# Kernel tuning notes

Hardware: AMD Instinct MI355X
Metric: run time of the kernel (lower is better)

Reference implementation:

```python
import jax, jax.numpy as jnp
import numpy as np

B, T, D, L = 64, 512, 1024, 32


def setup_inputs() -> dict:
    key = jax.random.key(0)
    ks = jax.random.split(key, 6)
    x = jax.random.normal(ks[0], (B, T, D), jnp.float32)
    W = jax.random.normal(ks[1], (D, L), jnp.float32) * 0.02  # TruncatedNormal(stddev=0.02) analogue
    b = jnp.zeros((L,), jnp.float32)
    transitions = jax.random.normal(ks[2], (L, L), jnp.float32) * 0.1
    label = jax.random.randint(ks[3], (B, T), 0, L).astype(jnp.int32)
    seqlen = jax.random.randint(ks[4], (B,), 1, T + 1).astype(jnp.int32)
    mask = jnp.arange(T)[None, :] < seqlen[:, None]
    return {"x": x, "W": W, "b": b, "transitions": transitions,
            "label": label, "seqlen": seqlen, "mask": mask}


def crf_sequence_score(emissions, label, seqlen, transitions):
    # emissions: [B,T,L]
    Bc, Tc, Lc = emissions.shape
    m = (jnp.arange(Tc)[None, :] < seqlen[:, None]).astype(emissions.dtype)  # [B,T]
    unary = jnp.take_along_axis(emissions, label[..., None].astype(jnp.int32), axis=-1)[..., 0]
    unary = jnp.sum(unary * m, axis=1)
    trans = transitions[label[:, :-1], label[:, 1:]]  # [B,T-1]
    mt = (jnp.arange(1, Tc)[None, :] < seqlen[:, None]).astype(emissions.dtype)
    binary = jnp.sum(trans * mt, axis=1)
    return unary + binary


def crf_log_norm(emissions, seqlen, transitions):
    Bc, Tc, Lc = emissions.shape
    alpha0 = emissions[:, 0]  # [B,L]
    valid = (jnp.arange(1, Tc)[None, :] < seqlen[:, None]).T  # [T-1,B]
    emits = jnp.moveaxis(emissions[:, 1:], 1, 0)  # [T-1,B,L]

    def step(alpha, inp):
        emit_t, v = inp
        new = jax.nn.logsumexp(alpha[:, :, None] + transitions[None], axis=1) + emit_t
        return jnp.where(v[:, None], new, alpha), None

    alpha, _ = jax.lax.scan(step, alpha0, (emits, valid))
    return jax.nn.logsumexp(alpha, axis=-1)  # [B]


def crf_decode(emissions, transitions, seqlen):
    Bc, Tc, Lc = emissions.shape
    alpha0 = emissions[:, 0]
    idx = jnp.arange(Lc, dtype=jnp.int32)
    valid = (jnp.arange(1, Tc)[None, :] < seqlen[:, None]).T  # [T-1,B]
    emits = jnp.moveaxis(emissions[:, 1:], 1, 0)

    def fwd(alpha, inp):
        emit_t, v = inp
        scores = alpha[:, :, None] + transitions[None]  # [B,L,L]
        best = jnp.max(scores, axis=1) + emit_t
        bp = jnp.argmax(scores, axis=1).astype(jnp.int32)  # [B,L]
        alpha_new = jnp.where(v[:, None], best, alpha)
        bp = jnp.where(v[:, None], bp, idx[None, :])  # identity bp on padded steps
        return alpha_new, bp

    alpha, bps = jax.lax.scan(fwd, alpha0, (emits, valid))  # bps: [T-1,B,L]
    last = jnp.argmax(alpha, axis=-1).astype(jnp.int32)  # [B]

    def bwd(tag, bp):
        prev = jnp.take_along_axis(bp, tag[:, None], axis=1)[:, 0]
        return prev, tag

    first, tags = jax.lax.scan(bwd, last, bps, reverse=True)  # tags[i] = tag at t=i+1
    seq = jnp.concatenate([first[None], tags], axis=0)  # [T,B]
    return jnp.moveaxis(seq, 0, 1)  # [B,T]


def reference(x, W, b, transitions, label, seqlen, mask):
    emissions = jnp.einsum('btd,dl->btl', x, W) + b  # Dense projection
    ll = crf_sequence_score(emissions, label, seqlen, transitions) - crf_log_norm(emissions, seqlen, transitions)
    loss = jnp.mean(-ll)
    vit = crf_decode(emissions, transitions, seqlen)
    tp = jnp.sum(((label > 0) & (vit == label)).astype(jnp.float32))
    tn = jnp.sum(((label > 0) & (vit != label)).astype(jnp.float32))
    fp = jnp.sum((mask & (label == 0) & (vit > 0)).astype(jnp.float32))
    return loss, vit, tp, tn, fp
```

## Files before the change

### kernel.cpp

```cpp
#include <hip/hip_runtime.h>
#include <stdint.h>
#include <math.h>

#define Bn 64
#define Tn 512
#define Dn 1024
#define Ln 32
#define LOG2E 1.4426950408889634f
#define LN2f  0.6931471805599453f

#define EMIS_OFF 0
#define LOGNORM_OFF (Bn * Tn * Ln)
#define SCORE_OFF (LOGNORM_OFF + Bn)
#define CNT_OFF (SCORE_OFF + Bn)

#define MAX3(a,b,c) fmaxf(fmaxf((a),(b)),(c))

__device__ __forceinline__ void half_swap(float p, float& x, float& y) {
    x = p; y = p;
    asm volatile("v_permlane32_swap_b32 %0, %1" : "+v"(x), "+v"(y));
}

#define BM 128
#define KB 32
#define XSS 132

__global__ __launch_bounds__(256) void gemm_emis(
    const float* __restrict__ x, const float* __restrict__ Wm,
    const float* __restrict__ bias, const int* __restrict__ seqlen,
    float* __restrict__ emis)
{
    int b  = blockIdx.x >> 2;
    int t0 = (blockIdx.x & 3) * BM;
    if (t0 >= seqlen[b]) return;

    __shared__ __align__(16) float xs[KB * XSS];
    __shared__ __align__(16) float wsh[KB * Ln];

    int tid = threadIdx.x;
    int cg = tid & 7;
    int rg = tid >> 3;

    const float* xrow = x + (size_t)(b * Tn + t0) * Dn;

    float acc[4][4];
    #pragma unroll
    for (int z = 0; z < 4; z++)
        #pragma unroll
        for (int c = 0; c < 4; c++) acc[z][c] = 0.f;

    float4 xr[4]; float4 wr;
    #pragma unroll
    for (int u = 0; u < 4; u++) {
        int f = tid + 256 * u;
        xr[u] = *(const float4*)(xrow + (size_t)(f >> 3) * Dn + (f & 7) * 4);
    }
    wr = *(const float4*)(Wm + tid * 4);

    for (int k0 = 0; k0 < Dn; k0 += KB) {
        __syncthreads();
        #pragma unroll
        for (int u = 0; u < 4; u++) {
            int f = tid + 256 * u;
            int lrow = f >> 3, kk = f & 7;
            xs[(4 * kk + 0) * XSS + lrow] = xr[u].x;
            xs[(4 * kk + 1) * XSS + lrow] = xr[u].y;
            xs[(4 * kk + 2) * XSS + lrow] = xr[u].z;
            xs[(4 * kk + 3) * XSS + lrow] = xr[u].w;
        }
        *(float4*)(wsh + tid * 4) = wr;
        __syncthreads();

        int kn = k0 + KB;
        if (kn < Dn) {
            #pragma unroll
            for (int u = 0; u < 4; u++) {
                int f = tid + 256 * u;
                xr[u] = *(const float4*)(xrow + (size_t)(f >> 3) * Dn + kn + (f & 7) * 4);
            }
            wr = *(const float4*)(Wm + (size_t)kn * Ln + tid * 4);
        }

        #pragma unroll 8
        for (int k = 0; k < KB; k++) {
            float4 a = *(const float4*)(xs + k * XSS + 4 * rg);
            float4 w = *(const float4*)(wsh + k * Ln + 4 * cg);
            float av[4] = {a.x, a.y, a.z, a.w};
            float wv[4] = {w.x, w.y, w.z, w.w};
            #pragma unroll
            for (int z = 0; z < 4; z++)
                #pragma unroll
                for (int c = 0; c < 4; c++)
                    acc[z][c] = fmaf(av[z], wv[c], acc[z][c]);
        }
    }

    float4 bv = *(const float4*)(bias + 4 * cg);
    float bb[4] = {bv.x, bv.y, bv.z, bv.w};
    #pragma unroll
    for (int z = 0; z < 4; z++) {
        float4 o;
        o.x = acc[z][0] + bb[0];
        o.y = acc[z][1] + bb[1];
        o.z = acc[z][2] + bb[2];
        o.w = acc[z][3] + bb[3];
        *(float4*)(emis + (size_t)(b * Tn + t0 + 4 * rg + z) * Ln + 4 * cg) = o;
    }
}

#define CH 64

__global__ __launch_bounds__(512) void crf_forward(
    const float* __restrict__ emis, const float* __restrict__ trans,
    const int* __restrict__ label, const int* __restrict__ seqlen,
    float* __restrict__ out, float* __restrict__ wsf)
{
    __shared__ __align__(16) float es[Tn * Ln];
    __shared__ __align__(16) float al[Tn * Ln];
    __shared__ __align__(16) float trs[Ln * Ln];
    __shared__ __align__(16) float abuf[64];
    __shared__ __align__(16) float lbuf[64];
    __shared__ uint8_t bp[Tn * Ln];
    __shared__ uint8_t Fm[16 * 32];
    __shared__ int btag[16];
    __shared__ int s_last;
    __shared__ float credA[8], credB[8], credC[8];

    int tid = threadIdx.x;
    int b = blockIdx.x;
    int slen = seqlen[b];
    int wv = tid >> 6;
    int lane = tid & 63;
    int j = lane & 31;
    int half = lane >> 5;

    const float* eb = emis + (size_t)b * Tn * Ln;

    {
        int n4 = slen * (Ln / 4);
        for (int i4 = tid; i4 < n4; i4 += 512)
            ((float4*)es)[i4] = ((const float4*)eb)[i4];
    }
    if (tid < 256) ((float4*)trs)[tid] = ((const float4*)trans)[tid];
    {
        uint32_t* bp32 = (uint32_t*)bp;
        for (int w = tid; w < Tn * Ln / 4; w += 512)
            bp32[w] = 0x03020100u + 0x04040404u * (uint32_t)(w & 7);
    }
    __syncthreads();

    float av = 0.f, emit = 0.f;
    float a = 0.f, eemit = 0.f;
    int   Eacc = 0;
    float tr[32];
    float e2[16];

    const int hoff = half ? 48 : 0;

    if (wv == 0) {
        #pragma unroll
        for (int i = 0; i < 16; i++) tr[i] = trs[(16 * half + i) * Ln + j];
        av = es[j];
        al[j] = av;
        emit = es[Ln + j];
    } else if (wv == 1) {
        #pragma unroll
        for (int i = 0; i < 16; i++) e2[i] = exp2f(trs[(16 * half + i) * Ln + j] * LOG2E);
        a = exp2f(es[j] * LOG2E);
        eemit = exp2f(es[Ln + j] * LOG2E);
    } else {
        #pragma unroll
        for (int i = 0; i < 32; i++) tr[i] = trs[i * Ln + j];
    }

    for (int c = 0; c < Tn / CH; c++) {
        int tb = (c == 0) ? 1 : c * CH;
        int te = (c + 1) * CH; if (te > slen) te = slen;

        if (wv == 0) {
            for (int t = tb; t < te; t++) {
                int tnx = (t + 1 < slen) ? (t + 1) : (slen - 1);
                float emitn = es[tnx * Ln + j];
                abuf[lane] = av;
                float4 A0 = *(const float4*)(abuf + hoff + 0);
                float4 A1 = *(const float4*)(abuf + hoff + 4);
                float4 A2 = *(const float4*)(abuf + hoff + 8);
                float4 A3 = *(const float4*)(abuf + hoff + 12);
                float vv[16];
                vv[0]=A0.x+tr[0];   vv[1]=A0.y+tr[1];   vv[2]=A0.z+tr[2];   vv[3]=A0.w+tr[3];
                vv[4]=A1.x+tr[4];   vv[5]=A1.y+tr[5];   vv[6]=A1.z+tr[6];   vv[7]=A1.w+tr[7];
                vv[8]=A2.x+tr[8];   vv[9]=A2.y+tr[9];   vv[10]=A2.z+tr[10]; vv[11]=A2.w+tr[11];
                vv[12]=A3.x+tr[12]; vv[13]=A3.y+tr[13]; vv[14]=A3.z+tr[14]; vv[15]=A3.w+tr[15];
                float g0 = MAX3(vv[0],  vv[1],  vv[2]);
                float g1 = MAX3(vv[3],  vv[4],  vv[5]);
                float g2 = MAX3(vv[6],  vv[7],  vv[8]);
                float g3 = MAX3(vv[9],  vv[10], vv[11]);
                float g4 = MAX3(vv[12], vv[13], vv[14]);
                float h0 = MAX3(g0, g1, g2);
                float h1 = MAX3(g3, g4, vv[15]);
                float p = fmaxf(h0, h1);
                float xx, yy;
                half_swap(p, xx, yy);
                av = fmaxf(xx, yy) + emit;
                al[t * Ln + j] = av;
                emit = emitn;
            }
        } else if (wv == 1) {
            for (int t = tb; t < te; t++) {
                int tnx = (t + 1 < slen) ? (t + 1) : (slen - 1);
                float emitn = es[tnx * Ln + j];
                lbuf[lane] = a;
                float4 A0 = *(const float4*)(lbuf + hoff + 0);
                float4 A1 = *(const float4*)(lbuf + hoff + 4);
                float4 A2 = *(const float4*)(lbuf + hoff + 8);
                float4 A3 = *(const float4*)(lbuf + hoff + 12);
                float eemitn = exp2f(emitn * LOG2E);
                float s0, s1, s2, s3;
                s0 = A0.x * e2[0];  s1 = A0.y * e2[1];  s2 = A0.z * e2[2];  s3 = A0.w * e2[3];
                s0 = fmaf(A1.x, e2[4],  s0); s1 = fmaf(A1.y, e2[5],  s1);
                s2 = fmaf(A1.z, e2[6],  s2); s3 = fmaf(A1.w, e2[7],  s3);
                s0 = fmaf(A2.x, e2[8],  s0); s1 = fmaf(A2.y, e2[9],  s1);
                s2 = fmaf(A2.z, e2[10], s2); s3 = fmaf(A2.w, e2[11], s3);
                s0 = fmaf(A3.x, e2[12], s0); s1 = fmaf(A3.y, e2[13], s1);
                s2 = fmaf(A3.z, e2[14], s2); s3 = fmaf(A3.w, e2[15], s3);
                float p = (s0 + s1) + (s2 + s3);
                float xx, yy;
                half_swap(p, xx, yy);
                float s = (xx + yy) * eemit;
                if ((t & 3) == 0) {
                    unsigned sb = (unsigned)__builtin_amdgcn_readfirstlane(__float_as_int(s));
                    int e = (int)((sb >> 23) & 0xFFu) - 127;
                    Eacc += e;
                    a = ldexpf(s, -e);
                } else {
                    a = s;
                }
                eemit = eemitn;
            }
        } else if (c == 0) {
            if (wv == 2) {
                const int* lb = label + (size_t)b * Tn;
                float acc = 0.f;
                for (int t = lane; t < Tn; t += 64) {
                    if (t < slen) {
                        int lc = lb[t];
                        acc += es[t * Ln + lc];
                        if (t >= 1) acc += trs[lb[t - 1] * Ln + lc];
                    }
                }
                #pragma unroll
                for (int off = 32; off >= 1; off >>= 1) acc += __shfl_xor(acc, off);
                if (lane == 0) wsf[SCORE_OFF + b] = acc;
            }
        } else {
            int stripe = (wv - 2) * 2 + (lane >> 5);
            int pb = ((c - 1) == 0) ? 1 : (c - 1) * CH;
            int pe = c * CH; if (pe > slen) pe = slen;
            for (int t = pb + stripe; t < pe; t += 12) {
                const float* ar = al + (t - 1) * Ln;
                float vv[32];
                #pragma unroll
                for (int i = 0; i < 32; i += 4) {
                    float4 a4 = *(const float4*)(ar + i);
                    vv[i]     = a4.x + tr[i];
                    vv[i + 1] = a4.y + tr[i + 1];
                    vv[i + 2] = a4.z + tr[i + 2];
                    vv[i + 3] = a4.w + tr[i + 3];
                }
                float mv[16]; int mi[16];
                #pragma unroll
                for (int i = 0; i < 16; i++) {
                    bool g = vv[2*i+1] > vv[2*i];
                    mv[i] = g ? vv[2*i+1] : vv[2*i];
                    mi[i] = g ? (2*i+1) : (2*i);
                }
                #pragma unroll
                for (int i = 0; i < 8; i++) {
                    bool g = mv[2*i+1] > mv[2*i];
                    mv[i] = g ? mv[2*i+1] : mv[2*i];
                    mi[i] = g ? mi[2*i+1] : mi[2*i];
                }
                #pragma unroll
                for (int i = 0; i < 4; i++) {
                    bool g = mv[2*i+1] > mv[2*i];
                    mv[i] = g ? mv[2*i+1] : mv[2*i];
                    mi[i] = g ? mi[2*i+1] : mi[2*i];
                }
                #pragma unroll
                for (int i = 0; i < 2; i++) {
                    bool g = mv[2*i+1] > mv[2*i];
                    mv[i] = g ? mv[2*i+1] : mv[2*i];
                    mi[i] = g ? mi[2*i+1] : mi[2*i];
                }
                bp[t * Ln + j] = (uint8_t)mi[0];
            }
        }
        __syncthreads();
    }

    if (wv == 0) {
        float mm = av; int ai = j;
        #pragma unroll
        for (int off = 16; off >= 1; off >>= 1) {
            float om = __shfl_xor(mm, off);
            int   oi = __shfl_xor(ai, off);
            if (om > mm || (om == mm && oi < ai)) { mm = om; ai = oi; }
        }
        if (lane == 0) s_last = ai;
    } else if (wv == 1) {
        float ss = a;
        #pragma unroll
        for (int off = 16; off >= 1; off >>= 1) ss += __shfl_xor(ss, off);
        if (lane == 0)
            wsf[LOGNORM_OFF + b] = fmaf(log2f(ss) + (float)Eacc, LN2f, 0.f);
    } else {
        int stripe = (wv - 2) * 2 + (lane >> 5);
        int cc = Tn / CH - 1;
        int pb = cc * CH;
        int pe = Tn; if (pe > slen) pe = slen;
        for (int t = pb + stripe; t < pe; t += 12) {
            const float* ar = al + (t - 1) * Ln;
            float vv[32];
            #pragma unroll
            for (int i = 0; i < 32; i += 4) {
                float4 a4 = *(const float4*)(ar + i);
                vv[i]     = a4.x + tr[i];
                vv[i + 1] = a4.y + tr[i + 1];
                vv[i + 2] = a4.z + tr[i + 2];
                vv[i + 3] = a4.w + tr[i + 3];
            }
            float mv[16]; int mi[16];
            #pragma unroll
            for (int i = 0; i < 16; i++) {
                bool g = vv[2*i+1] > vv[2*i];
                mv[i] = g ? vv[2*i+1] : vv[2*i];
                mi[i] = g ? (2*i+1) : (2*i);
            }
            #pragma unroll
            for (int i = 0; i < 8; i++) {
                bool g = mv[2*i+1] > mv[2*i];
                mv[i] = g ? mv[2*i+1] : mv[2*i];
                mi[i] = g ? mi[2*i+1] : mi[2*i];
            }
            #pragma unroll
            for (int i = 0; i < 4; i++) {
                bool g = mv[2*i+1] > mv[2*i];
                mv[i] = g ? mv[2*i+1] : mv[2*i];
                mi[i] = g ? mi[2*i+1] : mi[2*i];
            }
            #pragma unroll
            for (int i = 0; i < 2; i++) {
                bool g = mv[2*i+1] > mv[2*i];
                mv[i] = g ? mv[2*i+1] : mv[2*i];
                mi[i] = g ? mi[2*i+1] : mi[2*i];
            }
            bp[t * Ln + j] = (uint8_t)mi[0];
        }
    }
    __syncthreads();

    int sseg = tid >> 5, ent = tid & 31;
    {
        int y = ent;
        for (int p = 32 * sseg + 31; p >= 32 * sseg; p--) y = bp[p * Ln + y];
        Fm[sseg * 32 + ent] = (uint8_t)y;
    }
    __syncthreads();
    if (tid == 0) {
        int y = s_last;
        btag[15] = y;
        for (int ss = 15; ss >= 1; ss--) { y = Fm[ss * 32 + y]; btag[ss - 1] = y; }
    }
    __syncthreads();
    int q = tid;
    int y = btag[sseg];
    for (int p = 32 * sseg + 31; p >= q + 1; p--) y = bp[p * Ln + y];
    out[1 + (size_t)b * Tn + q] = (float)y;

    int lbl = label[(size_t)b * Tn + q];
    float tpf = (lbl > 0 && y == lbl) ? 1.f : 0.f;
    float tnf = (lbl > 0 && y != lbl) ? 1.f : 0.f;
    float fpf = (q < slen && lbl == 0 && y > 0) ? 1.f : 0.f;
    #pragma unroll
    for (int off = 32; off >= 1; off >>= 1) {
        tpf += __shfl_xor(tpf, off);
        tnf += __shfl_xor(tnf, off);
        fpf += __shfl_xor(fpf, off);
    }
    if (lane == 0) { credA[wv] = tpf; credB[wv] = tnf; credC[wv] = fpf; }
    __syncthreads();
    if (tid == 0) {
        float aa = 0.f, bb2 = 0.f, cc2 = 0.f;
        #pragma unroll
        for (int w = 0; w < 8; w++) { aa += credA[w]; bb2 += credB[w]; cc2 += credC[w]; }
        wsf[CNT_OFF + b] = aa;
        wsf[CNT_OFF + Bn + b] = bb2;
        wsf[CNT_OFF + 2 * Bn + b] = cc2;
    }
}

__global__ __launch_bounds__(64) void crf_final(const float* __restrict__ wsf,
                                                float* __restrict__ out)
{
    int lane = threadIdx.x;
    float nll = wsf[LOGNORM_OFF + lane] - wsf[SCORE_OFF + lane];
    float tp = wsf[CNT_OFF + lane];
    float tn = wsf[CNT_OFF + Bn + lane];
    float fp = wsf[CNT_OFF + 2 * Bn + lane];
    #pragma unroll
    for (int off = 32; off >= 1; off >>= 1) {
        nll += __shfl_xor(nll, off);
        tp  += __shfl_xor(tp, off);
        tn  += __shfl_xor(tn, off);
        fp  += __shfl_xor(fp, off);
    }
    if (lane == 0) {
        out[0] = nll * (1.f / 64.f);
        out[1 + Bn * Tn + 0] = tp;
        out[1 + Bn * Tn + 1] = tn;
        out[1 + Bn * Tn + 2] = fp;
    }
}

extern "C" void kernel_launch(void* const* d_in, const int* in_sizes, int n_in,
                              void* d_out, int out_size, void* d_ws, size_t ws_size,
                              hipStream_t stream) {
    const float* x     = (const float*)d_in[0];
    const float* W     = (const float*)d_in[1];
    const float* bias  = (const float*)d_in[2];
    const float* trans = (const float*)d_in[3];
    const int* label   = (const int*)d_in[4];
    const int* seqlen  = (const int*)d_in[5];
    float* out = (float*)d_out;
    float* wsf = (float*)d_ws;

    gemm_emis<<<dim3(Bn * (Tn / BM)), dim3(256), 0, stream>>>(x, W, bias, seqlen, wsf + EMIS_OFF);
    crf_forward<<<dim3(Bn), dim3(512), 0, stream>>>(wsf + EMIS_OFF, trans, label, seqlen, out, wsf);
    crf_final<<<dim3(1), dim3(64), 0, stream>>>(wsf, out);
}
```

Measured before the change: 295.0 us.

## Replace LDS alpha broadcast with DPP row rotations in CRF recurrences

The serial Viterbi and forward recurrences in waves 0 and 1 stop writing alpha to a shared buffer and reading it back as float4s each step. Instead, each lane gathers the sixteen predecessor values with DPP row-rotate moves, and the transition registers are reindexed to match the rotation order. A permlane16 swap then redistributes the result so every 16-lane row holds the values it needs next, which doubles the values held across the wave, so the final reductions span 64 lanes and the log-norm subtracts one. This targets the LDS round-trip latency on the critical serial path, at the cost of extra cross-lane instructions and more intricate lane mapping.

```diff
diff --git a/kernel.cpp b/kernel.cpp
--- a/kernel.cpp
+++ b/kernel.cpp
@@ -16,9 +16,27 @@
 
 #define MAX3(a,b,c) fmaxf(fmaxf((a),(b)),(c))
 
-__device__ __forceinline__ void half_swap(float p, float& x, float& y) {
-    x = p; y = p;
+template<int K>
+__device__ __forceinline__ float rorf(float v) {
+    return __int_as_float(__builtin_amdgcn_update_dpp(
+        0, __float_as_int(v), 0x120 | K, 0xF, 0xF, true));
+}
+
+__device__ __forceinline__ float opaque_copy(float v) {
+    float r;
+    asm volatile("v_mov_b32 %0, %1" : "=v"(r) : "v"(v));
+    return r;
+}
+
+__device__ __forceinline__ void swap32p(float p, float& x, float& y) {
+    x = p;
+    y = opaque_copy(p);
     asm volatile("v_permlane32_swap_b32 %0, %1" : "+v"(x), "+v"(y));
+}
+__device__ __forceinline__ void swap16p(float p, float& x, float& y) {
+    x = p;
+    y = opaque_copy(p);
+    asm volatile("v_permlane16_swap_b32 %0, %1" : "+v"(x), "+v"(y));
 }
 
 #define BM 128
@@ -118,8 +136,6 @@
     __shared__ __align__(16) float es[Tn * Ln];
     __shared__ __align__(16) float al[Tn * Ln];
     __shared__ __align__(16) float trs[Ln * Ln];
-    __shared__ __align__(16) float abuf[64];
-    __shared__ __align__(16) float lbuf[64];
     __shared__ uint8_t bp[Tn * Ln];
     __shared__ uint8_t Fm[16 * 32];
     __shared__ int btag[16];
@@ -132,7 +148,6 @@
     int wv = tid >> 6;
     int lane = tid & 63;
     int j = lane & 31;
-    int half = lane >> 5;
 
     const float* eb = emis + (size_t)b * Tn * Ln;
 
@@ -147,6 +162,30 @@
         for (int w = tid; w < Tn * Ln / 4; w += 512)
             bp32[w] = 0x03020100u + 0x04040404u * (uint32_t)(w & 7);
     }
+
+    int rq[16];
+    {
+        float qf = (float)(lane & 15);
+        rq[0]  = lane & 15;
+        rq[1]  = (int)rorf<1>(qf);   rq[2]  = (int)rorf<2>(qf);
+        rq[3]  = (int)rorf<3>(qf);   rq[4]  = (int)rorf<4>(qf);
+        rq[5]  = (int)rorf<5>(qf);   rq[6]  = (int)rorf<6>(qf);
+        rq[7]  = (int)rorf<7>(qf);   rq[8]  = (int)rorf<8>(qf);
+        rq[9]  = (int)rorf<9>(qf);   rq[10] = (int)rorf<10>(qf);
+        rq[11] = (int)rorf<11>(qf);  rq[12] = (int)rorf<12>(qf);
+        rq[13] = (int)rorf<13>(qf);  rq[14] = (int)rorf<14>(qf);
+        rq[15] = (int)rorf<15>(qf);
+    }
+    bool useX;
+    {
+        float px, py; swap16p((float)lane, px, py);
+        useX = (px == (float)(lane ^ 16));
+    }
+    int hoff = (lane & 32) ? 16 : 0;
+    int hidx = (lane & 15) + hoff;
+    int row2 = (lane >> 4) & 3;
+    bool keepC = (row2 == 0) || (row2 == 3);
+
     __syncthreads();
 
     float av = 0.f, emit = 0.f;
@@ -155,18 +194,16 @@
     float tr[32];
     float e2[16];
 
-    const int hoff = half ? 48 : 0;
-
     if (wv == 0) {
         #pragma unroll
-        for (int i = 0; i < 16; i++) tr[i] = trs[(16 * half + i) * Ln + j];
-        av = es[j];
-        al[j] = av;
+        for (int k = 0; k < 16; k++) tr[k] = trs[(rq[k] + hoff) * Ln + j];
+        av = es[hidx];
+        al[hidx] = av;
         emit = es[Ln + j];
     } else if (wv == 1) {
         #pragma unroll
-        for (int i = 0; i < 16; i++) e2[i] = exp2f(trs[(16 * half + i) * Ln + j] * LOG2E);
-        a = exp2f(es[j] * LOG2E);
+        for (int k = 0; k < 16; k++) e2[k] = exp2f(trs[(rq[k] + hoff) * Ln + j] * LOG2E);
+        a = exp2f(es[hidx] * LOG2E);
         eemit = exp2f(es[Ln + j] * LOG2E);
     } else {
         #pragma unroll
@@ -178,63 +215,79 @@
         int te = (c + 1) * CH; if (te > slen) te = slen;
 
         if (wv == 0) {
+            #pragma unroll 2
             for (int t = tb; t < te; t++) {
                 int tnx = (t + 1 < slen) ? (t + 1) : (slen - 1);
                 float emitn = es[tnx * Ln + j];
-                abuf[lane] = av;
-                float4 A0 = *(const float4*)(abuf + hoff + 0);
-                float4 A1 = *(const float4*)(abuf + hoff + 4);
-                float4 A2 = *(const float4*)(abuf + hoff + 8);
-                float4 A3 = *(const float4*)(abuf + hoff + 12);
-                float vv[16];
-                vv[0]=A0.x+tr[0];   vv[1]=A0.y+tr[1];   vv[2]=A0.z+tr[2];   vv[3]=A0.w+tr[3];
-                vv[4]=A1.x+tr[4];   vv[5]=A1.y+tr[5];   vv[6]=A1.z+tr[6];   vv[7]=A1.w+tr[7];
-                vv[8]=A2.x+tr[8];   vv[9]=A2.y+tr[9];   vv[10]=A2.z+tr[10]; vv[11]=A2.w+tr[11];
-                vv[12]=A3.x+tr[12]; vv[13]=A3.y+tr[13]; vv[14]=A3.z+tr[14]; vv[15]=A3.w+tr[15];
-                float g0 = MAX3(vv[0],  vv[1],  vv[2]);
-                float g1 = MAX3(vv[3],  vv[4],  vv[5]);
-                float g2 = MAX3(vv[6],  vv[7],  vv[8]);
-                float g3 = MAX3(vv[9],  vv[10], vv[11]);
-                float g4 = MAX3(vv[12], vv[13], vv[14]);
+                float vv0  = av           + tr[0];
+                float vv1  = rorf<1>(av)  + tr[1];
+                float vv2  = rorf<2>(av)  + tr[2];
+                float vv3  = rorf<3>(av)  + tr[3];
+                float vv4  = rorf<4>(av)  + tr[4];
+                float vv5  = rorf<5>(av)  + tr[5];
+                float vv6  = rorf<6>(av)  + tr[6];
+                float vv7  = rorf<7>(av)  + tr[7];
+                float vv8  = rorf<8>(av)  + tr[8];
+                float vv9  = rorf<9>(av)  + tr[9];
+                float vv10 = rorf<10>(av) + tr[10];
+                float vv11 = rorf<11>(av) + tr[11];
+                float vv12 = rorf<12>(av) + tr[12];
+                float vv13 = rorf<13>(av) + tr[13];
+                float vv14 = rorf<14>(av) + tr[14];
+                float vv15 = rorf<15>(av) + tr[15];
+                float g0 = MAX3(vv0,  vv1,  vv2);
+                float g1 = MAX3(vv3,  vv4,  vv5);
+                float g2 = MAX3(vv6,  vv7,  vv8);
+                float g3 = MAX3(vv9,  vv10, vv11);
+                float g4 = MAX3(vv12, vv13, vv14);
                 float h0 = MAX3(g0, g1, g2);
-                float h1 = MAX3(g3, g4, vv[15]);
+                float h1 = MAX3(g3, g4, vv15);
                 float p = fmaxf(h0, h1);
-                float xx, yy;
-                half_swap(p, xx, yy);
-                av = fmaxf(xx, yy) + emit;
-                al[t * Ln + j] = av;
+                float x, y; swap32p(p, x, y);
+                float cmb = fmaxf(x, y) + emit;
+                al[t * Ln + j] = cmb;
+                float x2, y2; swap16p(cmb, x2, y2);
+                float z = useX ? x2 : y2;
+                av = keepC ? cmb : z;
                 emit = emitn;
             }
         } else if (wv == 1) {
+            #pragma unroll 2
             for (int t = tb; t < te; t++) {
                 int tnx = (t + 1 < slen) ? (t + 1) : (slen - 1);
                 float emitn = es[tnx * Ln + j];
-                lbuf[lane] = a;
-                float4 A0 = *(const float4*)(lbuf + hoff + 0);
-                float4 A1 = *(const float4*)(lbuf + hoff + 4);
-                float4 A2 = *(const float4*)(lbuf + hoff + 8);
-                float4 A3 = *(const float4*)(lbuf + hoff + 12);
                 float eemitn = exp2f(emitn * LOG2E);
-                float s0, s1, s2, s3;
-                s0 = A0.x * e2[0];  s1 = A0.y * e2[1];  s2 = A0.z * e2[2];  s3 = A0.w * e2[3];
-                s0 = fmaf(A1.x, e2[4],  s0); s1 = fmaf(A1.y, e2[5],  s1);
-                s2 = fmaf(A1.z, e2[6],  s2); s3 = fmaf(A1.w, e2[7],  s3);
-                s0 = fmaf(A2.x, e2[8],  s0); s1 = fmaf(A2.y, e2[9],  s1);
-                s2 = fmaf(A2.z, e2[10], s2); s3 = fmaf(A2.w, e2[11], s3);
-                s0 = fmaf(A3.x, e2[12], s0); s1 = fmaf(A3.y, e2[13], s1);
-                s2 = fmaf(A3.z, e2[14], s2); s3 = fmaf(A3.w, e2[15], s3);
-                float p = (s0 + s1) + (s2 + s3);
-                float xx, yy;
-                half_swap(p, xx, yy);
-                float s = (xx + yy) * eemit;
+                float s0 = a           * e2[0];
+                float s1 = rorf<1>(a)  * e2[1];
+                float s2 = rorf<2>(a)  * e2[2];
+                float s3 = rorf<3>(a)  * e2[3];
+                s0 = fmaf(rorf<4>(a),  e2[4],  s0);
+                s1 = fmaf(rorf<5>(a),  e2[5],  s1);
+                s2 = fmaf(rorf<6>(a),  e2[6],  s2);
+                s3 = fmaf(rorf<7>(a),  e2[7],  s3);
+                s0 = fmaf(rorf<8>(a),  e2[8],  s0);
+                s1 = fmaf(rorf<9>(a),  e2[9],  s1);
+                s2 = fmaf(rorf<10>(a), e2[10], s2);
+                s3 = fmaf(rorf<11>(a), e2[11], s3);
+                s0 = fmaf(rorf<12>(a), e2[12], s0);
+                s1 = fmaf(rorf<13>(a), e2[13], s1);
+                s2 = fmaf(rorf<14>(a), e2[14], s2);
+                s3 = fmaf(rorf<15>(a), e2[15], s3);
+                float pp = (s0 + s1) + (s2 + s3);
+                float x, y; swap32p(pp, x, y);
+                float s = (x + y) * eemit;
+                float an;
                 if ((t & 3) == 0) {
                     unsigned sb = (unsigned)__builtin_amdgcn_readfirstlane(__float_as_int(s));
                     int e = (int)((sb >> 23) & 0xFFu) - 127;
                     Eacc += e;
-                    a = ldexpf(s, -e);
+                    an = ldexpf(s, -e);
                 } else {
-                    a = s;
-                }
+                    an = s;
+                }
+                float x2, y2; swap16p(an, x2, y2);
+                float z = useX ? x2 : y2;
+                a = keepC ? an : z;
                 eemit = eemitn;
             }
         } else if (c == 0) {
@@ -299,9 +352,9 @@
     }
 
     if (wv == 0) {
-        float mm = av; int ai = j;
-        #pragma unroll
-        for (int off = 16; off >= 1; off >>= 1) {
+        float mm = av; int ai = hidx;
+        #pragma unroll
+        for (int off = 32; off >= 1; off >>= 1) {
             float om = __shfl_xor(mm, off);
             int   oi = __shfl_xor(ai, off);
             if (om > mm || (om == mm && oi < ai)) { mm = om; ai = oi; }
@@ -310,9 +363,9 @@
     } else if (wv == 1) {
         float ss = a;
         #pragma unroll
-        for (int off = 16; off >= 1; off >>= 1) ss += __shfl_xor(ss, off);
+        for (int off = 32; off >= 1; off >>= 1) ss += __shfl_xor(ss, off);
         if (lane == 0)
-            wsf[LOGNORM_OFF + b] = fmaf(log2f(ss) + (float)Eacc, LN2f, 0.f);
+            wsf[LOGNORM_OFF + b] = (log2f(ss) - 1.0f + (float)Eacc) * LN2f;
     } else {
         int stripe = (wv - 2) * 2 + (lane >> 5);
         int cc = Tn / CH - 1;
```

After: 286.3 us. -2.9%, faster.
